# Kernel tuning notes

Measured on AMD Instinct MI355X. Metric: run time of the kernel, lower is better.

Reference implementation:

```python
import jax, jax.numpy as jnp
import numpy as np

B, S, D, L, R = 8, 128, 512, 512, 50  # batch, seq_len, input_dim, linear_dim, n_rel_labels


def _head_params(key, n_out):
    k1, k2, k3, k4 = jax.random.split(key, 4)
    s1 = 1.0 / np.sqrt(2 * D)
    s2 = 1.0 / np.sqrt(L)
    return (jax.random.uniform(k1, (2 * D, L), jnp.float32, -s1, s1),
            jax.random.uniform(k2, (L,), jnp.float32, -s1, s1),
            jax.random.uniform(k3, (L, n_out), jnp.float32, -s2, s2),
            jax.random.uniform(k4, (n_out,), jnp.float32, -s2, s2))


def setup_inputs() -> dict:
    key = jax.random.key(0)
    kx, ks, kh, kt, kl = jax.random.split(key, 5)
    x = jax.random.normal(kx, (B, S, D), jnp.float32)
    span = _head_params(ks, 1)
    h2h = _head_params(kh, 1)
    t2t = _head_params(kt, 1)
    lab = _head_params(kl, R)
    return {
        'x': x,
        'span_W1': span[0], 'span_b1': span[1], 'span_W2': span[2], 'span_b2': span[3],
        'h2h_W1': h2h[0], 'h2h_b1': h2h[1], 'h2h_W2': h2h[2], 'h2h_b2': h2h[3],
        't2t_W1': t2t[0], 't2t_b1': t2t[1], 't2t_W2': t2t[2], 't2t_b2': t2t[3],
        'lab_W1': lab[0], 'lab_b1': lab[1], 'lab_W2': lab[2], 'lab_b2': lab[3],
    }


def _pair_head(x, W1, b1, W2, b2):
    # Linear on concat([x_i, x_j]) == x_i @ W_left + x_j @ W_right  (avoids [B,S,S,2D] concat)
    d = x.shape[-1]
    Wl, Wr = W1[:d], W1[d:]
    left = jnp.einsum('bid,dl->bil', x, Wl)   # [B,S,L]
    right = jnp.einsum('bjd,dl->bjl', x, Wr)  # [B,S,L]
    h = jnp.tanh(left[:, :, None, :] + right[:, None, :, :] + b1)  # [B,S,S,L]
    return jnp.einsum('bijl,lo->bijo', h, W2) + b2  # [B,S,S,n_out]


def reference(x, span_W1, span_b1, span_W2, span_b2,
              h2h_W1, h2h_b1, h2h_W2, h2h_b2,
              t2t_W1, t2t_b1, t2t_W2, t2t_b2,
              lab_W1, lab_b1, lab_W2, lab_b2):
    shst = _pair_head(x, span_W1, span_b1, span_W2, span_b2)[..., 0]  # [B,S,S]
    # torch: movedim(-1,1) -> triu + triu(1).T -> movedim(1,-1)
    bt = jnp.swapaxes(shst, 1, 2)
    sym = jnp.triu(bt) + jnp.swapaxes(jnp.triu(bt, 1), -1, -2)
    shst = jnp.swapaxes(sym, 1, 2)
    shoh = _pair_head(x, h2h_W1, h2h_b1, h2h_W2, h2h_b2)[..., 0]
    stot = _pair_head(x, t2t_W1, t2t_b1, t2t_W2, t2t_b2)[..., 0]
    shoh_labels = _pair_head(x, lab_W1, lab_b1, lab_W2, lab_b2)  # [B,S,S,R]
    return (shst, shoh, stot, shoh_labels)
```

## Files before the change

### kernel.cpp

```cpp
#include <hip/hip_runtime.h>

#define Bsz 8
#define Ssz 128
#define Dsz 512
#define D2 1024
#define Lsz 512
#define Rsz 50
#define SLOT 524288
#define BSLOT 65536
#define OUTMAT 131072

typedef __attribute__((ext_vector_type(8))) _Float16 f16x8;
typedef __attribute__((ext_vector_type(2))) __fp16 fp16x2;
typedef __attribute__((ext_vector_type(4))) float f32x4;

union UV4 { uint4 u; f16x8 h; };
union UH { unsigned short s; _Float16 h; };
union UP { fp16x2 h; unsigned u; };

struct K1Args {
  const float* W1[4];
  const float* b1[4];
};

__device__ __forceinline__ float f16lo(unsigned u) {
  UH x; x.s = (unsigned short)(u & 0xffffu); return (float)x.h;
}
__device__ __forceinline__ float f16hi(unsigned u) {
  UH x; x.s = (unsigned short)(u >> 16); return (float)x.h;
}
__device__ __forceinline__ float f16v(unsigned short s) {
  UH x; x.s = s; return (float)x.h;
}
__device__ __forceinline__ unsigned pkrtz(float a, float b) {
  UP c; c.h = __builtin_amdgcn_cvt_pkrtz(a, b); return c.u;
}
__device__ __forceinline__ unsigned short f2h(float v) {
  UH x; x.h = (_Float16)v; return x.s;
}
__device__ __forceinline__ float rcpf(float x) {
  return __builtin_amdgcn_rcpf(x);
}

__global__ __launch_bounds__(256) void prep_all(
    const float* __restrict__ x, K1Args a, const float* __restrict__ W2,
    const float* __restrict__ w2a, const float* __restrict__ w2b,
    const float* __restrict__ w2c,
    const float* __restrict__ b2a, const float* __restrict__ b2b,
    const float* __restrict__ b2c,
    unsigned short* __restrict__ W1F, unsigned short* __restrict__ X16F,
    unsigned short* __restrict__ W2F, float* __restrict__ Sums) {
  const int z = blockIdx.z;
  const int t = threadIdx.x;
  if (z < 4) {
    if (blockIdx.x >= 8) return;
    __shared__ float S[64][65];
    const float* __restrict__ W = a.W1[z];
    const int n0 = blockIdx.x * 64;
    const int k0 = blockIdx.y * 64;
    {
      const int kk = t >> 2, c16 = (t & 3) * 16;
      const float* p = W + (k0 + kk) * Lsz + n0 + c16;
#pragma unroll
      for (int c = 0; c < 4; ++c) {
        float4 v = *(const float4*)(p + c * 4);
        S[kk][c16 + c * 4 + 0] = v.x; S[kk][c16 + c * 4 + 1] = v.y;
        S[kk][c16 + c * 4 + 2] = v.z; S[kk][c16 + c * 4 + 3] = v.w;
      }
    }
    __syncthreads();
#pragma unroll
    for (int o = t; o < 512; o += 256) {
      const int lane = o & 63;
      const int ntl = (o >> 6) & 3, kbl = o >> 8;
      const int n_l = ntl * 16 + (lane & 15);
      const int k_l = kbl * 32 + (lane >> 4) * 8;
      uint4 pk;
      pk.x = pkrtz(S[k_l + 0][n_l], S[k_l + 1][n_l]);
      pk.y = pkrtz(S[k_l + 2][n_l], S[k_l + 3][n_l]);
      pk.z = pkrtz(S[k_l + 4][n_l], S[k_l + 5][n_l]);
      pk.w = pkrtz(S[k_l + 6][n_l], S[k_l + 7][n_l]);
      const long addr =
          ((long)((z * 32 + blockIdx.x * 4 + ntl) * 32 + blockIdx.y * 2 + kbl) *
               64 + lane) * 8;
      *(uint4*)(W1F + addr) = pk;
    }
  } else if (z == 4) {
    if (blockIdx.x >= 16) return;
    const int idx = (blockIdx.y * 16 + blockIdx.x) * 256 + t;
    const int frag = idx >> 6, lane = idx & 63;
    const int m = (frag >> 4) * 16 + (lane & 15);
    const int k0 = (frag & 15) * 32 + (lane >> 4) * 8;
    const float* p = x + m * Dsz + k0;
    float4 v0 = *(const float4*)p, v1 = *(const float4*)(p + 4);
    uint4 pk = make_uint4(pkrtz(v0.x, v0.y), pkrtz(v0.z, v0.w),
                          pkrtz(v1.x, v1.y), pkrtz(v1.z, v1.w));
    *(uint4*)(X16F + (long)idx * 8) = pk;
  } else {
    if (blockIdx.y != 0) return;
    if (blockIdx.x < 16) {
      const int idx = blockIdx.x * 256 + t;
      const int frag = idx >> 6, lane = idx & 63;
      const int o = (frag >> 4) * 16 + (lane & 15);
      const int k0 = (frag & 15) * 32 + (lane >> 4) * 8;
      float v[8];
#pragma unroll
      for (int e = 0; e < 8; ++e)
        v[e] = (o < Rsz) ? W2[(k0 + e) * Rsz + o] : 0.0f;
      uint4 pk = make_uint4(pkrtz(v[0], v[1]), pkrtz(v[2], v[3]),
                            pkrtz(v[4], v[5]), pkrtz(v[6], v[7]));
      *(uint4*)(W2F + (long)idx * 8) = pk;
    } else if (blockIdx.x < 19) {
      const int h = blockIdx.x - 16;
      const float* __restrict__ w2 = (h == 0) ? w2a : (h == 1 ? w2b : w2c);
      const float bb = (h == 0) ? b2a[0] : (h == 1 ? b2b[0] : b2c[0]);
      __shared__ float red[256];
      red[t] = w2[t] + w2[t + 256];
      __syncthreads();
      for (int s = 128; s > 0; s >>= 1) {
        if (t < s) red[t] += red[t + s];
        __syncthreads();
      }
      if (t == 0) Sums[h] = red[0] + bb;
    }
  }
}

__global__ __launch_bounds__(256) void gemm_lr_f16f(
    const unsigned short* __restrict__ X16F,
    const unsigned short* __restrict__ W1F, K1Args a,
    unsigned short* __restrict__ U) {
  const int side = blockIdx.z;
  const int h = side >> 1, r = side & 1;
  const float* __restrict__ bias = a.b1[h];
  const int tid = threadIdx.x;
  const int w = tid >> 6, lane = tid & 63;
  const int lm = lane & 15, q = lane >> 4;
  const int mtb = blockIdx.y * 4 + (w & 1) * 2;
  const int ntb = blockIdx.x * 4 + (w >> 1) * 2;

  f32x4 acc[2][2];
#pragma unroll
  for (int mt = 0; mt < 2; ++mt)
#pragma unroll
    for (int nt = 0; nt < 2; ++nt) {
      acc[mt][nt].x = 0.f; acc[mt][nt].y = 0.f;
      acc[mt][nt].z = 0.f; acc[mt][nt].w = 0.f;
    }

  for (int kb = 0; kb < 16; ++kb) {
    UV4 af[2], bf[2];
#pragma unroll
    for (int mt = 0; mt < 2; ++mt)
      af[mt].u = *(const uint4*)(X16F +
          ((long)((mtb + mt) * 16 + kb) * 64 + lane) * 8);
#pragma unroll
    for (int nt = 0; nt < 2; ++nt)
      bf[nt].u = *(const uint4*)(W1F +
          ((long)((h * 32 + ntb + nt) * 32 + r * 16 + kb) * 64 + lane) * 8);
#pragma unroll
    for (int mt = 0; mt < 2; ++mt)
#pragma unroll
      for (int nt = 0; nt < 2; ++nt)
        acc[mt][nt] = __builtin_amdgcn_mfma_f32_16x16x32_f16(
            af[mt].h, bf[nt].h, acc[mt][nt], 0, 0, 0);
  }

  unsigned short* slot = U + side * SLOT;
  if (h < 3) {
#pragma unroll
    for (int nt = 0; nt < 2; ++nt) {
      const int n_out = (ntb + nt) * 16 + lm;
      const float bb = (r == 0) ? bias[n_out] : 0.0f;
#pragma unroll
      for (int mt = 0; mt < 2; ++mt) {
        const int m0r = (mtb + mt) * 16 + q * 4;
        const float e0 = __expf(2.0f * (acc[mt][nt].x + bb));
        const float e1 = __expf(2.0f * (acc[mt][nt].y + bb));
        const float e2 = __expf(2.0f * (acc[mt][nt].z + bb));
        const float e3 = __expf(2.0f * (acc[mt][nt].w + bb));
        uint2 pr;
        pr.x = pkrtz(e0, e1);
        pr.y = pkrtz(e2, e3);
        const int bi = m0r >> 7, il = m0r & 127;
        *(uint2*)(slot + bi * BSLOT + n_out * Ssz + il) = pr;
      }
    }
  } else {
#pragma unroll
    for (int nt = 0; nt < 2; ++nt) {
      const int n_out = (ntb + nt) * 16 + lm;
      const float bb = (r == 0) ? bias[n_out] : 0.0f;
#pragma unroll
      for (int mt = 0; mt < 2; ++mt) {
#pragma unroll
        for (int reg = 0; reg < 4; ++reg) {
          const int m_out = (mtb + mt) * 16 + q * 4 + reg;
          float v;
          if (reg == 0) v = acc[mt][nt].x;
          else if (reg == 1) v = acc[mt][nt].y;
          else if (reg == 2) v = acc[mt][nt].z;
          else v = acc[mt][nt].w;
          slot[m_out * Lsz + n_out] = f2h(__expf(2.0f * (v + bb)));
        }
      }
    }
  }
}

__global__ __launch_bounds__(256) void pair_fused(
    const unsigned short* __restrict__ U,
    const unsigned short* __restrict__ W2F,
    const float* __restrict__ b2l,
    const float* __restrict__ w2a, const float* __restrict__ w2b,
    const float* __restrict__ w2c, const float* __restrict__ Sums,
    float* __restrict__ out) {
  __shared__ union __align__(16) {
    struct { unsigned short Rs[2][128][68];
             unsigned short Bs[2][8][512]; }
        L;
    struct { unsigned short As[64][20];
             unsigned short Bs[64][40];
             float w2s[64]; }
        S;
  } sm;

  const int b = blockIdx.y;
  const int tid = threadIdx.x;

  if ((blockIdx.x & 1) == 0) {
    const int i = blockIdx.x >> 1;
    const int w = tid >> 6, lane = tid & 63;
    const int lm = lane & 15, q = lane >> 4;
    const int jb = w * 32;

    const unsigned short* __restrict__ Lrow =
        U + 6 * SLOT + (b * Ssz + i) * Lsz;
    const unsigned short* __restrict__ Rb0 = U + 7 * SLOT + (long)b * Ssz * Lsz;
    float* out3 = out + 3 * OUTMAT;

    const int sr = tid >> 1;
    const int sh = (tid & 1) * 32;
    const unsigned short* Rg = Rb0 + sr * Lsz + sh;
    const int bfrag = tid >> 5;
    const int bo = (tid & 31) * 16;
    const int fragN = (bfrag & 3) * 16 + (bfrag >> 2);

    f32x4 acc[2][4];
#pragma unroll
    for (int mt = 0; mt < 2; ++mt)
#pragma unroll
      for (int nt = 0; nt < 4; ++nt) {
        acc[mt][nt].x = 0.f; acc[mt][nt].y = 0.f;
        acc[mt][nt].z = 0.f; acc[mt][nt].w = 0.f;
      }

    uint4 rp0, rp1, rp2, rp3, bp0, bp1;
    {
      const unsigned short* p = Rg;
      rp0 = *(const uint4*)(p);      rp1 = *(const uint4*)(p + 8);
      rp2 = *(const uint4*)(p + 16); rp3 = *(const uint4*)(p + 24);
      const unsigned short* bp = W2F + (long)fragN * 512 + bo;
      bp0 = *(const uint4*)(bp);     bp1 = *(const uint4*)(bp + 8);
    }
    *(uint4*)&sm.L.Rs[0][sr][sh + 0]  = rp0;
    *(uint4*)&sm.L.Rs[0][sr][sh + 8]  = rp1;
    *(uint4*)&sm.L.Rs[0][sr][sh + 16] = rp2;
    *(uint4*)&sm.L.Rs[0][sr][sh + 24] = rp3;
    *(uint4*)&sm.L.Bs[0][bfrag][bo]     = bp0;
    *(uint4*)&sm.L.Bs[0][bfrag][bo + 8] = bp1;
    __syncthreads();

#pragma unroll 1
    for (int c = 0; c < 8; ++c) {
      const int buf = c & 1;
      if (c < 7) {
        const unsigned short* p = Rg + (c + 1) * 64;
        rp0 = *(const uint4*)(p);      rp1 = *(const uint4*)(p + 8);
        rp2 = *(const uint4*)(p + 16); rp3 = *(const uint4*)(p + 24);
        const unsigned short* bp = W2F + (long)(fragN + (c + 1) * 2) * 512 + bo;
        bp0 = *(const uint4*)(bp);     bp1 = *(const uint4*)(bp + 8);
      }
      const uint4 lf0 = *(const uint4*)(Lrow + c * 64 + q * 8);
      const uint4 lf1 = *(const uint4*)(Lrow + c * 64 + 32 + q * 8);

#pragma unroll
      for (int kbl = 0; kbl < 2; ++kbl) {
        const uint4 lf = kbl ? lf1 : lf0;
        float ea[8];
        ea[0] = f16lo(lf.x); ea[1] = f16hi(lf.x);
        ea[2] = f16lo(lf.y); ea[3] = f16hi(lf.y);
        ea[4] = f16lo(lf.z); ea[5] = f16hi(lf.z);
        ea[6] = f16lo(lf.w); ea[7] = f16hi(lf.w);
        UV4 bfr[4];
#pragma unroll
        for (int nt = 0; nt < 4; ++nt)
          bfr[nt].u = *(const uint4*)&sm.L.Bs[buf][kbl * 4 + nt][lane * 8];
#pragma unroll
        for (int mt = 0; mt < 2; ++mt) {
          const uint4 rv =
              *(const uint4*)&sm.L.Rs[buf][jb + mt * 16 + lm][kbl * 32 + q * 8];
          float eb[8];
          eb[0] = f16lo(rv.x); eb[1] = f16hi(rv.x);
          eb[2] = f16lo(rv.y); eb[3] = f16hi(rv.y);
          eb[4] = f16lo(rv.z); eb[5] = f16hi(rv.z);
          eb[6] = f16lo(rv.w); eb[7] = f16hi(rv.w);
          float hh[8];
#pragma unroll
          for (int e = 0; e < 8; ++e)
            hh[e] = fmaf(-2.0f, rcpf(fmaf(ea[e], eb[e], 1.0f)), 1.0f);
          UV4 A;
          A.u = make_uint4(pkrtz(hh[0], hh[1]), pkrtz(hh[2], hh[3]),
                           pkrtz(hh[4], hh[5]), pkrtz(hh[6], hh[7]));
#pragma unroll
          for (int nt = 0; nt < 4; ++nt)
            acc[mt][nt] = __builtin_amdgcn_mfma_f32_16x16x32_f16(
                A.h, bfr[nt].h, acc[mt][nt], 0, 0, 0);
        }
      }
      if (c < 7) {
        const int nb = buf ^ 1;
        *(uint4*)&sm.L.Rs[nb][sr][sh + 0]  = rp0;
        *(uint4*)&sm.L.Rs[nb][sr][sh + 8]  = rp1;
        *(uint4*)&sm.L.Rs[nb][sr][sh + 16] = rp2;
        *(uint4*)&sm.L.Rs[nb][sr][sh + 24] = rp3;
        *(uint4*)&sm.L.Bs[nb][bfrag][bo]     = bp0;
        *(uint4*)&sm.L.Bs[nb][bfrag][bo + 8] = bp1;
      }
      __syncthreads();
    }

#pragma unroll
    for (int nt = 0; nt < 4; ++nt) {
      const int o = nt * 16 + lm;
      if (o >= Rsz) continue;
      const float bias = b2l[o];
#pragma unroll
      for (int mt = 0; mt < 2; ++mt) {
#pragma unroll
        for (int reg = 0; reg < 4; ++reg) {
          const int j = jb + mt * 16 + q * 4 + reg;
          const long base = ((long)((b * Ssz + i) * Ssz) + j) * Rsz;
          float v;
          if (reg == 0) v = acc[mt][nt].x;
          else if (reg == 1) v = acc[mt][nt].y;
          else if (reg == 2) v = acc[mt][nt].z;
          else v = acc[mt][nt].w;
          out3[base + o] = v + bias;
        }
      }
    }
  } else {
    const int s = blockIdx.x >> 1;
    if (s >= 96) return;
    const int h = s >> 5;
    const int r = s & 31;
    const int it = r >> 2, jt = r & 3;
    const int i0 = it * 16, j0 = jt * 32;
    if (h == 0 && i0 + 15 < j0) return;
    const int t = tid;
    const int tj = t & 31;
    const int th = t >> 5;

    const unsigned short* __restrict__ A  = U + (2 * h) * SLOT + b * BSLOT;
    const unsigned short* __restrict__ Bt = U + (2 * h + 1) * SLOT + b * BSLOT;
    const float* __restrict__ w2 = (h == 0) ? w2a : (h == 1 ? w2b : w2c);

    float acc0 = 0.f, acc1 = 0.f;
    const int sr = t >> 2;
    const int scA = (t & 3) * 4;
    const int scB = (t & 3) * 8;

    for (int lc = 0; lc < Lsz; lc += 64) {
      __syncthreads();
      *(uint2*)&sm.S.As[sr][scA] =
          *(const uint2*)(A + (lc + sr) * Ssz + i0 + scA);
      *(uint4*)&sm.S.Bs[sr][scB] =
          *(const uint4*)(Bt + (lc + sr) * Ssz + j0 + scB);
      if (t < 64) sm.S.w2s[t] = w2[lc + t];
      __syncthreads();
#pragma unroll 8
      for (int l = 0; l < 64; ++l) {
        const float wv = sm.S.w2s[l];
        const unsigned ua = *(const unsigned*)&sm.S.As[l][th * 2];
        const float a0 = f16lo(ua), a1 = f16hi(ua);
        const float bb = f16v(sm.S.Bs[l][tj]);
        acc0 = fmaf(wv, rcpf(fmaf(a0, bb, 1.0f)), acc0);
        acc1 = fmaf(wv, rcpf(fmaf(a1, bb, 1.0f)), acc1);
      }
    }

    const float Sh = Sums[h];
    const float v0 = fmaf(-2.0f, acc0, Sh);
    const float v1 = fmaf(-2.0f, acc1, Sh);
    const int i = i0 + th * 2, j = j0 + tj;
    if (h == 0) {
      if (j <= i) {
        out[(b * Ssz + i) * Ssz + j] = v0;
        out[(b * Ssz + j) * Ssz + i] = v0;
      }
      if (j <= i + 1) {
        out[(b * Ssz + i + 1) * Ssz + j] = v1;
        out[(b * Ssz + j) * Ssz + (i + 1)] = v1;
      }
    } else {
      float* o = out + h * OUTMAT;
      o[(b * Ssz + i) * Ssz + j] = v0;
      o[(b * Ssz + i + 1) * Ssz + j] = v1;
    }
  }
}

extern "C" void kernel_launch(void* const* d_in, const int* in_sizes, int n_in,
                              void* d_out, int out_size, void* d_ws,
                              size_t ws_size, hipStream_t stream) {
  (void)in_sizes; (void)n_in; (void)out_size; (void)ws_size;
  const float* x = (const float*)d_in[0];
  K1Args a;
  a.W1[0] = (const float*)d_in[1];  a.b1[0] = (const float*)d_in[2];
  a.W1[1] = (const float*)d_in[5];  a.b1[1] = (const float*)d_in[6];
  a.W1[2] = (const float*)d_in[9];  a.b1[2] = (const float*)d_in[10];
  a.W1[3] = (const float*)d_in[13]; a.b1[3] = (const float*)d_in[14];
  const float* w2a = (const float*)d_in[3];
  const float* b2a = (const float*)d_in[4];
  const float* w2b = (const float*)d_in[7];
  const float* b2b = (const float*)d_in[8];
  const float* w2c = (const float*)d_in[11];
  const float* b2c = (const float*)d_in[12];
  const float* W2l = (const float*)d_in[15];
  const float* b2l = (const float*)d_in[16];
  float* out = (float*)d_out;

  unsigned short* U    = (unsigned short*)d_ws;
  unsigned short* W1F  = U + 8 * SLOT;
  unsigned short* X16F = U + 8 * SLOT + 4 * (Lsz * D2);
  unsigned short* W2F  = U + 8 * SLOT + 5 * (Lsz * D2);
  float* Sums = (float*)(W2F + 64 * Lsz);

  prep_all<<<dim3(19, 16, 6), 256, 0, stream>>>(
      x, a, W2l, w2a, w2b, w2c, b2a, b2b, b2c, W1F, X16F, W2F, Sums);
  gemm_lr_f16f<<<dim3(8, 16, 8), 256, 0, stream>>>(X16F, W1F, a, U);
  pair_fused<<<dim3(256, Bsz), 256, 0, stream>>>(
      U, W2F, b2l, w2a, w2b, w2c, Sums, out);
}
```

Baseline: 164.3 us.

## Read label-head R and W2 fragments directly from global memory instead of LDS staging

The label-head branch of pair_fused no longer double-buffers the R rows and W2 fragments through shared memory with per-chunk barriers. Each lane now loads its MFMA operands straight from global memory (relying on L1/L2 reuse), and the chunk loop is unrolled by 2. The shared-memory union shrinks to the small scalar-head buffers, which lowers LDS use per block and may allow more resident blocks. The cost is redundant global/cache traffic, since the four waves re-read the same W2 fragments, and the loss of explicit prefetch overlap.

Measured after the change: 165.4 us. About the same (+0.7%).

```diff
diff --git a/kernel.cpp b/kernel.cpp
--- a/kernel.cpp
+++ b/kernel.cpp
@@ -215,15 +215,9 @@
     const float* __restrict__ w2a, const float* __restrict__ w2b,
     const float* __restrict__ w2c, const float* __restrict__ Sums,
     float* __restrict__ out) {
-  __shared__ union __align__(16) {
-    struct { unsigned short Rs[2][128][68];
-             unsigned short Bs[2][8][512]; }
-        L;
-    struct { unsigned short As[64][20];
-             unsigned short Bs[64][40];
-             float w2s[64]; }
-        S;
-  } sm;
+  __shared__ unsigned short As[64][20];
+  __shared__ unsigned short Bs[64][40];
+  __shared__ float w2s[64];
 
   const int b = blockIdx.y;
   const int tid = threadIdx.x;
@@ -239,12 +233,10 @@
     const unsigned short* __restrict__ Rb0 = U + 7 * SLOT + (long)b * Ssz * Lsz;
     float* out3 = out + 3 * OUTMAT;
 
-    const int sr = tid >> 1;
-    const int sh = (tid & 1) * 32;
-    const unsigned short* Rg = Rb0 + sr * Lsz + sh;
-    const int bfrag = tid >> 5;
-    const int bo = (tid & 31) * 16;
-    const int fragN = (bfrag & 3) * 16 + (bfrag >> 2);
+    const unsigned short* Lb = Lrow + q * 8;
+    const unsigned short* R0 = Rb0 + (jb + lm) * Lsz + q * 8;
+    const unsigned short* R1 = Rb0 + (jb + 16 + lm) * Lsz + q * 8;
+    const unsigned short* Bb = W2F + lane * 8;
 
     f32x4 acc[2][4];
 #pragma unroll
@@ -255,35 +247,10 @@
         acc[mt][nt].z = 0.f; acc[mt][nt].w = 0.f;
       }
 
-    uint4 rp0, rp1, rp2, rp3, bp0, bp1;
-    {
-      const unsigned short* p = Rg;
-      rp0 = *(const uint4*)(p);      rp1 = *(const uint4*)(p + 8);
-      rp2 = *(const uint4*)(p + 16); rp3 = *(const uint4*)(p + 24);
-      const unsigned short* bp = W2F + (long)fragN * 512 + bo;
-      bp0 = *(const uint4*)(bp);     bp1 = *(const uint4*)(bp + 8);
-    }
-    *(uint4*)&sm.L.Rs[0][sr][sh + 0]  = rp0;
-    *(uint4*)&sm.L.Rs[0][sr][sh + 8]  = rp1;
-    *(uint4*)&sm.L.Rs[0][sr][sh + 16] = rp2;
-    *(uint4*)&sm.L.Rs[0][sr][sh + 24] = rp3;
-    *(uint4*)&sm.L.Bs[0][bfrag][bo]     = bp0;
-    *(uint4*)&sm.L.Bs[0][bfrag][bo + 8] = bp1;
-    __syncthreads();
-
-#pragma unroll 1
+#pragma unroll 2
     for (int c = 0; c < 8; ++c) {
-      const int buf = c & 1;
-      if (c < 7) {
-        const unsigned short* p = Rg + (c + 1) * 64;
-        rp0 = *(const uint4*)(p);      rp1 = *(const uint4*)(p + 8);
-        rp2 = *(const uint4*)(p + 16); rp3 = *(const uint4*)(p + 24);
-        const unsigned short* bp = W2F + (long)(fragN + (c + 1) * 2) * 512 + bo;
-        bp0 = *(const uint4*)(bp);     bp1 = *(const uint4*)(bp + 8);
-      }
-      const uint4 lf0 = *(const uint4*)(Lrow + c * 64 + q * 8);
-      const uint4 lf1 = *(const uint4*)(Lrow + c * 64 + 32 + q * 8);
-
+      const uint4 lf0 = *(const uint4*)(Lb + c * 64);
+      const uint4 lf1 = *(const uint4*)(Lb + c * 64 + 32);
 #pragma unroll
       for (int kbl = 0; kbl < 2; ++kbl) {
         const uint4 lf = kbl ? lf1 : lf0;
@@ -295,11 +262,12 @@
         UV4 bfr[4];
 #pragma unroll
         for (int nt = 0; nt < 4; ++nt)
-          bfr[nt].u = *(const uint4*)&sm.L.Bs[buf][kbl * 4 + nt][lane * 8];
+          bfr[nt].u =
+              *(const uint4*)(Bb + (long)(nt * 16 + kbl + 2 * c) * 512);
 #pragma unroll
         for (int mt = 0; mt < 2; ++mt) {
           const uint4 rv =
-              *(const uint4*)&sm.L.Rs[buf][jb + mt * 16 + lm][kbl * 32 + q * 8];
+              *(const uint4*)((mt ? R1 : R0) + c * 64 + kbl * 32);
           float eb[8];
           eb[0] = f16lo(rv.x); eb[1] = f16hi(rv.x);
           eb[2] = f16lo(rv.y); eb[3] = f16hi(rv.y);
@@ -318,16 +286,6 @@
                 A.h, bfr[nt].h, acc[mt][nt], 0, 0, 0);
         }
       }
-      if (c < 7) {
-        const int nb = buf ^ 1;
-        *(uint4*)&sm.L.Rs[nb][sr][sh + 0]  = rp0;
-        *(uint4*)&sm.L.Rs[nb][sr][sh + 8]  = rp1;
-        *(uint4*)&sm.L.Rs[nb][sr][sh + 16] = rp2;
-        *(uint4*)&sm.L.Rs[nb][sr][sh + 24] = rp3;
-        *(uint4*)&sm.L.Bs[nb][bfrag][bo]     = bp0;
-        *(uint4*)&sm.L.Bs[nb][bfrag][bo + 8] = bp1;
-      }
-      __syncthreads();
     }
 
 #pragma unroll
@@ -373,18 +331,16 @@
 
     for (int lc = 0; lc < Lsz; lc += 64) {
       __syncthreads();
-      *(uint2*)&sm.S.As[sr][scA] =
-          *(const uint2*)(A + (lc + sr) * Ssz + i0 + scA);
-      *(uint4*)&sm.S.Bs[sr][scB] =
-          *(const uint4*)(Bt + (lc + sr) * Ssz + j0 + scB);
-      if (t < 64) sm.S.w2s[t] = w2[lc + t];
+      *(uint2*)&As[sr][scA] = *(const uint2*)(A + (lc + sr) * Ssz + i0 + scA);
+      *(uint4*)&Bs[sr][scB] = *(const uint4*)(Bt + (lc + sr) * Ssz + j0 + scB);
+      if (t < 64) w2s[t] = w2[lc + t];
       __syncthreads();
 #pragma unroll 8
       for (int l = 0; l < 64; ++l) {
-        const float wv = sm.S.w2s[l];
-        const unsigned ua = *(const unsigned*)&sm.S.As[l][th * 2];
+        const float wv = w2s[l];
+        const unsigned ua = *(const unsigned*)&As[l][th * 2];
         const float a0 = f16lo(ua), a1 = f16hi(ua);
-        const float bb = f16v(sm.S.Bs[l][tj]);
+        const float bb = f16v(Bs[l][tj]);
         acc0 = fmaf(wv, rcpf(fmaf(a0, bb, 1.0f)), acc0);
         acc1 = fmaf(wv, rcpf(fmaf(a1, bb, 1.0f)), acc1);
       }
```
